# Performance work log

Measured on AMD Instinct MI355X. Metric: run time of the kernel, lower is better.

The kernel has to match this reference:

```python
import jax, jax.numpy as jnp
import numpy as np

B, S, D, E, H = 4, 4096, 1024, 8, 128  # batch, seq, d_model, experts, expert hidden (hardcoded 128)


def setup_inputs() -> dict:
    key = jax.random.key(0)
    ks = jax.random.split(key, 7)
    s_in = 1.0 / np.sqrt(D)
    s_h = 1.0 / np.sqrt(H)
    return {
        "x": jax.random.normal(ks[0], (B, S, D), dtype=jnp.float32),
        "W1": jax.random.normal(ks[1], (E, D, H), dtype=jnp.float32) * s_in,
        "b1": jax.random.normal(ks[2], (E, H), dtype=jnp.float32) * s_in,
        "W2": jax.random.normal(ks[3], (E, H, D), dtype=jnp.float32) * s_h,
        "b2": jax.random.normal(ks[4], (E, D), dtype=jnp.float32) * s_h,
        "Wg": jax.random.normal(ks[5], (D, E), dtype=jnp.float32) * s_in,
        "bg": jax.random.normal(ks[6], (E,), dtype=jnp.float32) * s_in,
    }


def reference(x, W1, b1, W2, b2, Wg, bg):
    # Gate: softmax over experts. [B,S,E]
    gate = jax.nn.softmax(jnp.einsum("bsd,de->bse", x, Wg) + bg, axis=-1)
    # Dense per-expert MLP applied to every token.
    h = jax.nn.relu(jnp.einsum("bsd,edh->bseh", x, W1) + b1)          # [B,S,E,H]
    y = jnp.einsum("bseh,eho->bseo", h, W2) + b2                       # [B,S,E,D]
    # Fused weighted sum over the expert axis (replaces the python double loop).
    out = jnp.einsum("bse,bseo->bso", gate, y)                         # [B,S,D]
    return out
```

## Files before the change

kernel.cpp:

```cpp
#include <hip/hip_runtime.h>
#include <hip/hip_bf16.h>

#define B_ 4
#define S_ 4096
#define D_ 1024
#define E_ 8
#define H_ 128
#define M_ (B_*S_)
#define K_ 1024
#define N_ 1024
#define NT_ (K_/64)
#define NIT_ (NT_/2)

typedef short bf16x8 __attribute__((ext_vector_type(8)));
typedef float f32x4 __attribute__((ext_vector_type(4)));

__device__ __forceinline__ unsigned short f2bf(float f){
  union { float f; unsigned int u; } v; v.f = f;
  unsigned int u = v.u;
  unsigned int r = (u + 0x7fffu + ((u >> 16) & 1u)) >> 16;
  return (unsigned short)r;
}

__device__ __forceinline__ void gload16(const void* g, void* l){
  __builtin_amdgcn_global_load_lds((const __attribute__((address_space(1))) void*)g,
                                   (__attribute__((address_space(3))) void*)l, 16, 0, 0);
}

__global__ __launch_bounds__(256)
void prep_x_gate(const float* __restrict__ x, const float* __restrict__ Wg,
                 const float* __restrict__ bg, unsigned short* __restrict__ xb,
                 float* __restrict__ gate){
  int tid = threadIdx.x;
  int lane = tid & 63;
  int m = blockIdx.x * 4 + (tid >> 6);
  const float* xr = x + (size_t)m * D_;
  unsigned short* xbr = xb + (size_t)m * D_;
  float acc[E_];
  #pragma unroll
  for (int e = 0; e < E_; ++e) acc[e] = 0.f;
  #pragma unroll
  for (int c = 0; c < D_/64; ++c){
    int d = c*64 + lane;
    float xs = xr[d];
    xbr[d] = f2bf(xs);
    const float4 w0 = *(const float4*)(Wg + (size_t)d * E_);
    const float4 w1 = *(const float4*)(Wg + (size_t)d * E_ + 4);
    acc[0] = fmaf(xs, w0.x, acc[0]); acc[1] = fmaf(xs, w0.y, acc[1]);
    acc[2] = fmaf(xs, w0.z, acc[2]); acc[3] = fmaf(xs, w0.w, acc[3]);
    acc[4] = fmaf(xs, w1.x, acc[4]); acc[5] = fmaf(xs, w1.y, acc[5]);
    acc[6] = fmaf(xs, w1.z, acc[6]); acc[7] = fmaf(xs, w1.w, acc[7]);
  }
  #pragma unroll
  for (int off = 32; off > 0; off >>= 1){
    #pragma unroll
    for (int e = 0; e < E_; ++e) acc[e] += __shfl_xor(acc[e], off, 64);
  }
  float lg[E_]; float mx = -1e30f;
  #pragma unroll
  for (int e = 0; e < E_; ++e){ lg[e] = acc[e] + bg[e]; mx = fmaxf(mx, lg[e]); }
  float s = 0.f;
  #pragma unroll
  for (int e = 0; e < E_; ++e){ lg[e] = expf(lg[e] - mx); s += lg[e]; }
  float inv = 1.f / s;
  if (lane < E_) gate[(size_t)m * E_ + lane] = lg[lane] * inv;
}

__global__ __launch_bounds__(256)
void transpose_pack(const float* __restrict__ in, unsigned short* __restrict__ out,
                    int C, int ostride, int in_estride, int out_ebase){
  __shared__ float t[32][33];
  int e = blockIdx.z;
  const float* ip = in + (size_t)e * in_estride;
  unsigned short* op = out + (size_t)e * out_ebase;
  int tx = threadIdx.x, ty = threadIdx.y;
  int c0 = blockIdx.x * 32, r0 = blockIdx.y * 32;
  #pragma unroll
  for (int yy = 0; yy < 32; yy += 8)
    t[ty + yy][tx] = ip[(size_t)(r0 + ty + yy) * C + (c0 + tx)];
  __syncthreads();
  #pragma unroll
  for (int yy = 0; yy < 32; yy += 8)
    op[(size_t)(c0 + ty + yy) * ostride + (r0 + tx)] = f2bf(t[tx][ty + yy]);
}

#define READ_A(b,r) do{ int ab_ = (b)*16384 + abase0; \
  _Pragma("unroll") for (int f2 = 0; f2 < 4; ++f2){ \
    af[f2][0] = *(const bf16x8*)&lds[ab_ + ((r)*4+f2)*1024 + bk0]; \
    af[f2][1] = *(const bf16x8*)&lds[ab_ + ((r)*4+f2)*1024 + bk1]; } }while(0)
#define READ_B(b,c) do{ int bb_ = (b)*16384 + bbase0; \
  _Pragma("unroll") for (int j2 = 0; j2 < 2; ++j2){ \
    bfr[(c)*2+j2][0] = *(const bf16x8*)&lds[bb_ + ((c)*2+j2)*1024 + bk0]; \
    bfr[(c)*2+j2][1] = *(const bf16x8*)&lds[bb_ + ((c)*2+j2)*1024 + bk1]; } }while(0)
#define MFMA16(r,c) do{ \
  _Pragma("unroll") for (int f2 = 0; f2 < 4; ++f2) \
  _Pragma("unroll") for (int j2 = 0; j2 < 2; ++j2){ \
    acc[(r)*4+f2][(c)*2+j2] = __builtin_amdgcn_mfma_f32_16x16x32_bf16(af[f2][0], bfr[(c)*2+j2][0], acc[(r)*4+f2][(c)*2+j2], 0,0,0); \
    acc[(r)*4+f2][(c)*2+j2] = __builtin_amdgcn_mfma_f32_16x16x32_bf16(af[f2][1], bfr[(c)*2+j2][1], acc[(r)*4+f2][(c)*2+j2], 0,0,0); \
  } }while(0)
#define PH_MID  __builtin_amdgcn_s_barrier(); \
                __builtin_amdgcn_s_setprio(1)
#define PH_END  __builtin_amdgcn_s_setprio(0)
#define VMW(N)  asm volatile("s_waitcnt vmcnt(" #N ")" ::: "memory")

template<int PASS>
__global__ __launch_bounds__(512, 2)
void gemm_moe8(const unsigned short* __restrict__ A,
               const unsigned short* __restrict__ Bt,
               const float* __restrict__ gate,
               const float* __restrict__ bias,
               void* __restrict__ outp)
{
  __shared__ unsigned short lds[65536];

  int bid = blockIdx.x;
  int xcd = bid & 7, pos = bid >> 3;
  int mb = xcd * 8 + (pos >> 2);
  int nb = pos & 3;
  int m0 = mb * 256, n0 = nb * 256;

  int tid = threadIdx.x;
  int lane = tid & 63;
  int w = tid >> 6;
  int wm = w & 1, wn = w >> 1;
  int rowi = lane & 15, s4 = lane >> 4;

  int sg = (tid & 7) ^ ((tid >> 3) & 7);
  const unsigned short* gA = A  + (size_t)(m0 + (tid >> 3)) * K_ + sg * 8;
  const unsigned short* gB = Bt + (size_t)(n0 + (tid >> 3)) * K_ + sg * 8;
  int t8 = tid * 8;

#define STAGE_A(b,h,kt) do{ const unsigned short* g_ = gA + (size_t)((h)*128)*K_ + (kt)*64; \
  gload16(g_,                 &lds[(b)*16384 + (h)*8192 + t8]); \
  gload16(g_ + (size_t)64*K_, &lds[(b)*16384 + (h)*8192 + t8 + 4096]); }while(0)
#define STAGE_B(b,h,kt) do{ const unsigned short* g_ = gB + (size_t)((h)*128)*K_ + (kt)*64; \
  gload16(g_,                 &lds[32768 + (b)*16384 + (h)*8192 + t8]); \
  gload16(g_ + (size_t)64*K_, &lds[32768 + (b)*16384 + (h)*8192 + t8 + 4096]); }while(0)

  int bk0 = rowi*64 + (( s4     ) ^ (rowi & 7)) * 8;
  int bk1 = rowi*64 + ((4 + s4  ) ^ (rowi & 7)) * 8;
  int abase0 = wm * 8192;
  int bbase0 = 32768 + (wn >> 1) * 8192 + (wn & 1) * 4096;

  f32x4 acc[8][4];
  #pragma unroll
  for (int i = 0; i < 8; ++i){
    #pragma unroll
    for (int j = 0; j < 4; ++j){ f32x4 z = {0.f,0.f,0.f,0.f}; acc[i][j] = z; }
  }
  bf16x8 af[4][2], bfr[4][2];

  STAGE_B(0,0,0); STAGE_B(0,1,0);
  STAGE_A(0,0,0); STAGE_A(0,1,0);
  STAGE_B(1,0,1); STAGE_B(1,1,1);
  STAGE_A(1,0,1);
  VMW(6);
  __builtin_amdgcn_s_barrier();

  #pragma unroll 1
  for (int it = 0; it < NIT_; ++it){
    int kt1  = 2*it + 1;
    int ktn0 = 2*it + 2, ktn1 = 2*it + 3;
    bool more = (it < NIT_ - 1);
    STAGE_A(1,1,kt1);
    READ_A(0,0); READ_B(0,0); READ_B(0,1);
    PH_MID; MFMA16(0,0); MFMA16(0,1); PH_END;
    READ_A(0,1);
    if (more){ STAGE_B(0,0,ktn0); STAGE_B(0,1,ktn0); VMW(4); }
    else     { VMW(0); }
    PH_MID; MFMA16(1,0); MFMA16(1,1); PH_END;
    READ_A(1,0); READ_B(1,0); READ_B(1,1);
    if (more){ STAGE_A(0,0,ktn0); STAGE_A(0,1,ktn0); }
    PH_MID; MFMA16(0,0); MFMA16(0,1); PH_END;
    READ_A(1,1);
    if (more){ STAGE_B(1,0,ktn1); STAGE_B(1,1,ktn1); STAGE_A(1,0,ktn1); }
    VMW(6);
    PH_MID; MFMA16(1,1); MFMA16(1,0); PH_END;
  }

  int ncol0 = n0 + wn*64;
  if (PASS == 1){
    __builtin_amdgcn_s_barrier();
    unsigned short* Hp = (unsigned short*)outp;
    float* lws = (float*)lds + w * 4096;
    int e = nb*2 + (wn >> 1);
    float b1v[4];
    #pragma unroll
    for (int j = 0; j < 4; ++j) b1v[j] = bias[e*H_ + (wn&1)*64 + j*16 + rowi];
    #pragma unroll
    for (int ci = 0; ci < 2; ++ci){
      #pragma unroll
      for (int f2 = 0; f2 < 4; ++f2){
        int fi = ci*4 + f2;
        #pragma unroll
        for (int jj = 0; jj < 4; ++jj){
          int m = m0 + wm*128 + fi*16 + s4*4 + jj;
          float g = gate[(size_t)m*E_ + e];
          int r_l = f2*16 + s4*4 + jj;
          #pragma unroll
          for (int j = 0; j < 4; ++j){
            float v = fmaxf(acc[fi][j][jj] + b1v[j], 0.f) * g;
            lws[r_l*64 + ((j*16 + rowi) ^ (s4 << 4))] = v;
          }
        }
      }
      asm volatile("s_waitcnt lgkmcnt(0)" ::: "memory");
      #pragma unroll
      for (int it2 = 0; it2 < 16; ++it2){
        int r_l = it2*4 + (lane >> 4);
        int c4  = lane & 15;
        int X2  = it2 & 3;
        f32x4 v = *(const f32x4*)&lws[r_l*64 + ((c4*4) ^ (X2 << 4))];
        union { unsigned short us[4]; uint2 u2; } pk;
        #pragma unroll
        for (int q = 0; q < 4; ++q) pk.us[q] = f2bf(v[q]);
        int m = m0 + wm*128 + ci*64 + r_l;
        *(uint2*)&Hp[(size_t)m*N_ + ncol0 + c4*4] = pk.u2;
      }
      if (ci == 0) asm volatile("s_waitcnt lgkmcnt(0)" ::: "memory");
    }
  } else {
    float* Out = (float*)outp;
    float b2v[8][4];
    #pragma unroll
    for (int j = 0; j < 4; ++j){
      int n = ncol0 + j*16 + rowi;
      #pragma unroll
      for (int e = 0; e < 8; ++e) b2v[e][j] = bias[(size_t)e*N_ + n];
    }
    #pragma unroll
    for (int fi = 0; fi < 8; ++fi){
      #pragma unroll
      for (int jj = 0; jj < 4; ++jj){
        int m = m0 + wm*128 + fi*16 + s4*4 + jj;
        const float4 g0 = *(const float4*)(gate + (size_t)m*E_);
        const float4 g1 = *(const float4*)(gate + (size_t)m*E_ + 4);
        float bv[4];
        #pragma unroll
        for (int j = 0; j < 4; ++j)
          bv[j] = g0.x*b2v[0][j] + g0.y*b2v[1][j] + g0.z*b2v[2][j] + g0.w*b2v[3][j]
                + g1.x*b2v[4][j] + g1.y*b2v[5][j] + g1.z*b2v[6][j] + g1.w*b2v[7][j];
        #pragma unroll
        for (int j = 0; j < 4; ++j)
          Out[(size_t)m*N_ + ncol0 + j*16 + rowi] = acc[fi][j][jj] + bv[j];
      }
    }
  }
#undef STAGE_A
#undef STAGE_B
}

extern "C" void kernel_launch(void* const* d_in, const int* in_sizes, int n_in,
                              void* d_out, int out_size, void* d_ws, size_t ws_size,
                              hipStream_t stream){
  const float* x  = (const float*)d_in[0];
  const float* W1 = (const float*)d_in[1];
  const float* b1 = (const float*)d_in[2];
  const float* W2 = (const float*)d_in[3];
  const float* b2 = (const float*)d_in[4];
  const float* Wg = (const float*)d_in[5];
  const float* bg = (const float*)d_in[6];
  float* out = (float*)d_out;

  char* ws = (char*)d_ws;
  unsigned short* xb  = (unsigned short*)(ws);
  unsigned short* Hp  = (unsigned short*)(ws + ((size_t)32<<20));
  unsigned short* B1T = (unsigned short*)(ws + ((size_t)64<<20));
  unsigned short* B2T = (unsigned short*)(ws + ((size_t)66<<20));
  float*          gate= (float*)(ws + ((size_t)68<<20));

  hipLaunchKernelGGL(prep_x_gate, dim3(M_/4), dim3(256), 0, stream, x, Wg, bg, xb, gate);
  hipLaunchKernelGGL(transpose_pack, dim3(128/32, 1024/32, 8), dim3(32,8), 0, stream,
                     W1, B1T, 128, 1024, 1024*128, 128*1024);
  hipLaunchKernelGGL(transpose_pack, dim3(1024/32, 128/32, 8), dim3(32,8), 0, stream,
                     W2, B2T, 1024, 1024, 128*1024, 128);
  hipLaunchKernelGGL((gemm_moe8<1>), dim3(256), dim3(512), 0, stream,
                     xb, B1T, gate, b1, (void*)Hp);
  hipLaunchKernelGGL((gemm_moe8<2>), dim3(256), dim3(512), 0, stream,
                     Hp, B2T, gate, b2, (void*)out);
}
```

Measured before the change: 101.4 us.

## Fuse both MoE GEMM passes into one cooperative kernel with per-row-block flags

Merges the two GEMM launches into a single cooperative kernel. Each block computes its first-layer tile, writes it to the hidden buffer, then waits on an atomic counter until all four N-blocks of its row block are done before running the second GEMM. This removes one kernel launch and the full-grid boundary between the passes, so row blocks can start the second GEMM as soon as their own dependencies finish. It adds a memset, atomics and spin-waiting, and relies on cooperative launch so all 256 blocks are co-resident.

```diff
diff --git a/kernel.cpp b/kernel.cpp
--- a/kernel.cpp
+++ b/kernel.cpp
@@ -103,32 +103,18 @@
 #define PH_END  __builtin_amdgcn_s_setprio(0)
 #define VMW(N)  asm volatile("s_waitcnt vmcnt(" #N ")" ::: "memory")
 
-template<int PASS>
-__global__ __launch_bounds__(512, 2)
-void gemm_moe8(const unsigned short* __restrict__ A,
-               const unsigned short* __restrict__ Bt,
-               const float* __restrict__ gate,
-               const float* __restrict__ bias,
-               void* __restrict__ outp)
+__device__ __forceinline__ void gemm_core(const unsigned short* __restrict__ A,
+                                          const unsigned short* __restrict__ Bt,
+                                          unsigned short* lds,
+                                          int m0, int n0, int tid,
+                                          int bk0, int bk1, int abase0, int bbase0,
+                                          f32x4 (&acc)[8][4])
 {
-  __shared__ unsigned short lds[65536];
-
-  int bid = blockIdx.x;
-  int xcd = bid & 7, pos = bid >> 3;
-  int mb = xcd * 8 + (pos >> 2);
-  int nb = pos & 3;
-  int m0 = mb * 256, n0 = nb * 256;
-
-  int tid = threadIdx.x;
-  int lane = tid & 63;
-  int w = tid >> 6;
-  int wm = w & 1, wn = w >> 1;
-  int rowi = lane & 15, s4 = lane >> 4;
-
   int sg = (tid & 7) ^ ((tid >> 3) & 7);
   const unsigned short* gA = A  + (size_t)(m0 + (tid >> 3)) * K_ + sg * 8;
   const unsigned short* gB = Bt + (size_t)(n0 + (tid >> 3)) * K_ + sg * 8;
   int t8 = tid * 8;
+  bf16x8 af[4][2], bfr[4][2];
 
 #define STAGE_A(b,h,kt) do{ const unsigned short* g_ = gA + (size_t)((h)*128)*K_ + (kt)*64; \
   gload16(g_,                 &lds[(b)*16384 + (h)*8192 + t8]); \
@@ -136,19 +122,6 @@
 #define STAGE_B(b,h,kt) do{ const unsigned short* g_ = gB + (size_t)((h)*128)*K_ + (kt)*64; \
   gload16(g_,                 &lds[32768 + (b)*16384 + (h)*8192 + t8]); \
   gload16(g_ + (size_t)64*K_, &lds[32768 + (b)*16384 + (h)*8192 + t8 + 4096]); }while(0)
-
-  int bk0 = rowi*64 + (( s4     ) ^ (rowi & 7)) * 8;
-  int bk1 = rowi*64 + ((4 + s4  ) ^ (rowi & 7)) * 8;
-  int abase0 = wm * 8192;
-  int bbase0 = 32768 + (wn >> 1) * 8192 + (wn & 1) * 4096;
-
-  f32x4 acc[8][4];
-  #pragma unroll
-  for (int i = 0; i < 8; ++i){
-    #pragma unroll
-    for (int j = 0; j < 4; ++j){ f32x4 z = {0.f,0.f,0.f,0.f}; acc[i][j] = z; }
-  }
-  bf16x8 af[4][2], bfr[4][2];
 
   STAGE_B(0,0,0); STAGE_B(0,1,0);
   STAGE_A(0,0,0); STAGE_A(0,1,0);
@@ -177,16 +150,57 @@
     VMW(6);
     PH_MID; MFMA16(1,1); MFMA16(1,0); PH_END;
   }
-
+#undef STAGE_A
+#undef STAGE_B
+}
+
+__global__ __launch_bounds__(512, 2)
+void moe_fused(const unsigned short* __restrict__ xb,
+               const unsigned short* __restrict__ B1T,
+               const unsigned short* __restrict__ B2T,
+               const float* __restrict__ gate,
+               const float* __restrict__ b1,
+               const float* __restrict__ b2,
+               unsigned short* __restrict__ Hp,
+               float* __restrict__ Out,
+               unsigned int* __restrict__ flags)
+{
+  __shared__ unsigned short lds[65536];
+
+  int bid = blockIdx.x;
+  int xcd = bid & 7, pos = bid >> 3;
+  int mb = xcd * 8 + (pos >> 2);
+  int nb = pos & 3;
+  int m0 = mb * 256, n0 = nb * 256;
+
+  int tid = threadIdx.x;
+  int lane = tid & 63;
+  int w = tid >> 6;
+  int wm = w & 1, wn = w >> 1;
+  int rowi = lane & 15, s4 = lane >> 4;
+
+  int bk0 = rowi*64 + (( s4     ) ^ (rowi & 7)) * 8;
+  int bk1 = rowi*64 + ((4 + s4  ) ^ (rowi & 7)) * 8;
+  int abase0 = wm * 8192;
+  int bbase0 = 32768 + (wn >> 1) * 8192 + (wn & 1) * 4096;
   int ncol0 = n0 + wn*64;
-  if (PASS == 1){
+
+  f32x4 acc[8][4];
+  #pragma unroll
+  for (int i = 0; i < 8; ++i){
+    #pragma unroll
+    for (int j = 0; j < 4; ++j){ f32x4 z = {0.f,0.f,0.f,0.f}; acc[i][j] = z; }
+  }
+
+  gemm_core(xb, B1T, lds, m0, n0, tid, bk0, bk1, abase0, bbase0, acc);
+
+  {
     __builtin_amdgcn_s_barrier();
-    unsigned short* Hp = (unsigned short*)outp;
     float* lws = (float*)lds + w * 4096;
     int e = nb*2 + (wn >> 1);
     float b1v[4];
     #pragma unroll
-    for (int j = 0; j < 4; ++j) b1v[j] = bias[e*H_ + (wn&1)*64 + j*16 + rowi];
+    for (int j = 0; j < 4; ++j) b1v[j] = b1[e*H_ + (wn&1)*64 + j*16 + rowi];
     #pragma unroll
     for (int ci = 0; ci < 2; ++ci){
       #pragma unroll
@@ -219,14 +233,32 @@
       }
       if (ci == 0) asm volatile("s_waitcnt lgkmcnt(0)" ::: "memory");
     }
-  } else {
-    float* Out = (float*)outp;
+  }
+
+  __threadfence();
+  __syncthreads();
+  if (tid == 0){
+    __hip_atomic_fetch_add(&flags[mb], 1u, __ATOMIC_ACQ_REL, __HIP_MEMORY_SCOPE_AGENT);
+    while (__hip_atomic_load(&flags[mb], __ATOMIC_ACQUIRE, __HIP_MEMORY_SCOPE_AGENT) < 4u)
+      __builtin_amdgcn_s_sleep(8);
+  }
+  __syncthreads();
+  __threadfence();
+
+  #pragma unroll
+  for (int i = 0; i < 8; ++i){
+    #pragma unroll
+    for (int j = 0; j < 4; ++j){ f32x4 z = {0.f,0.f,0.f,0.f}; acc[i][j] = z; }
+  }
+  gemm_core(Hp, B2T, lds, m0, n0, tid, bk0, bk1, abase0, bbase0, acc);
+
+  {
     float b2v[8][4];
     #pragma unroll
     for (int j = 0; j < 4; ++j){
       int n = ncol0 + j*16 + rowi;
       #pragma unroll
-      for (int e = 0; e < 8; ++e) b2v[e][j] = bias[(size_t)e*N_ + n];
+      for (int e = 0; e < 8; ++e) b2v[e][j] = b2[(size_t)e*N_ + n];
     }
     #pragma unroll
     for (int fi = 0; fi < 8; ++fi){
@@ -246,8 +278,6 @@
       }
     }
   }
-#undef STAGE_A
-#undef STAGE_B
 }
 
 extern "C" void kernel_launch(void* const* d_in, const int* in_sizes, int n_in,
@@ -263,19 +293,22 @@
   float* out = (float*)d_out;
 
   char* ws = (char*)d_ws;
-  unsigned short* xb  = (unsigned short*)(ws);
-  unsigned short* Hp  = (unsigned short*)(ws + ((size_t)32<<20));
-  unsigned short* B1T = (unsigned short*)(ws + ((size_t)64<<20));
-  unsigned short* B2T = (unsigned short*)(ws + ((size_t)66<<20));
-  float*          gate= (float*)(ws + ((size_t)68<<20));
-
+  unsigned short* xb   = (unsigned short*)(ws);
+  unsigned short* Hp   = (unsigned short*)(ws + ((size_t)32<<20));
+  unsigned short* B1T  = (unsigned short*)(ws + ((size_t)64<<20));
+  unsigned short* B2T  = (unsigned short*)(ws + ((size_t)66<<20));
+  float*          gate = (float*)(ws + ((size_t)68<<20));
+  unsigned int*   flags= (unsigned int*)(ws + ((size_t)69<<20));
+
+  hipMemsetAsync(flags, 0, 64 * sizeof(unsigned int), stream);
   hipLaunchKernelGGL(prep_x_gate, dim3(M_/4), dim3(256), 0, stream, x, Wg, bg, xb, gate);
   hipLaunchKernelGGL(transpose_pack, dim3(128/32, 1024/32, 8), dim3(32,8), 0, stream,
                      W1, B1T, 128, 1024, 1024*128, 128*1024);
   hipLaunchKernelGGL(transpose_pack, dim3(1024/32, 128/32, 8), dim3(32,8), 0, stream,
                      W2, B2T, 1024, 1024, 128*1024, 128);
-  hipLaunchKernelGGL((gemm_moe8<1>), dim3(256), dim3(512), 0, stream,
-                     xb, B1T, gate, b1, (void*)Hp);
-  hipLaunchKernelGGL((gemm_moe8<2>), dim3(256), dim3(512), 0, stream,
-                     Hp, B2T, gate, b2, (void*)out);
-}
+
+  void* kargs[] = { (void*)&xb, (void*)&B1T, (void*)&B2T, (void*)&gate,
+                    (void*)&b1, (void*)&b2, (void*)&Hp, (void*)&out, (void*)&flags };
+  hipLaunchCooperativeKernel((const void*)moe_fused, dim3(256), dim3(512),
+                             kargs, 0, stream);
+}
```

New measurement: 220.4 us. +117.4%, slower.
